# Kernel tuning notes

Hardware: AMD Instinct MI355X
Metric: run time of the kernel (lower is better)

The kernel has to match this reference:

```python
import jax, jax.numpy as jnp
import numpy as np

N_NODES = 50000
N_EDGES = 500000
D = 128
R = 8
L = 2
BN_EPS = 1e-5


def setup_inputs() -> dict:
    key = jax.random.key(0)
    ks = jax.random.split(key, 8)
    x = jax.random.normal(ks[0], (N_NODES, D), dtype=jnp.float32)
    xe = jax.random.normal(ks[1], (N_EDGES, D), dtype=jnp.float32)
    edge_index = jax.random.randint(ks[2], (2, N_EDGES), 0, N_NODES, dtype=jnp.int64)
    edge_type = jax.random.randint(ks[3], (N_EDGES,), 0, R, dtype=jnp.int64)
    # glorot init for weight/root, zeros bias; BN affine params
    w_scale = jnp.sqrt(6.0 / (D + D))
    weight = jax.random.uniform(ks[4], (L, R, D, D), jnp.float32, -w_scale, w_scale)
    root = jax.random.uniform(ks[5], (L, D, D), jnp.float32, -w_scale, w_scale)
    bias = jnp.zeros((L, D), jnp.float32)
    bn_gamma = jnp.ones((L, D), jnp.float32)
    bn_beta = jnp.zeros((L, D), jnp.float32)
    return {"x": x, "xe": xe, "edge_index": edge_index, "edge_type": edge_type,
            "weight": weight, "root": root, "bias": bias,
            "bn_gamma": bn_gamma, "bn_beta": bn_beta}


def _rgcn_edge_conv(h, xe, src, dst, etype, w, rt, b):
    # message: relu(x_j + xe) per edge (independent of relation mask)
    m = jax.nn.relu(h[src] + xe)                         # [E, D]
    # mean-aggregate per (relation, dst) via a combined segment id
    n = h.shape[0]
    seg = etype * n + dst                                # [E]
    sums = jax.ops.segment_sum(m, seg, num_segments=R * n)            # [R*N, D]
    cnt = jax.ops.segment_sum(jnp.ones((m.shape[0],), m.dtype), seg,
                              num_segments=R * n)                     # [R*N]
    mean = sums / jnp.maximum(cnt, 1.0)[:, None]
    hr = mean.reshape(R, n, -1)                          # [R, N, D]
    out = jnp.einsum('rnd,rdo->no', hr, w)               # sum_i H_i @ W_i
    out = out + h @ rt + b
    return out


def _batch_norm(h, gamma, beta):
    mu = h.mean(axis=0)
    var = jnp.mean((h - mu) ** 2, axis=0)  # biased, as torch BN (training)
    return (h - mu) * jax.lax.rsqrt(var + BN_EPS) * gamma + beta


def reference(x, xe, edge_index, edge_type, weight, root, bias, bn_gamma, bn_beta):
    src, dst = edge_index[0], edge_index[1]
    h = x
    for l in range(L):
        h = _rgcn_edge_conv(h, xe, src, dst, edge_type, weight[l], root[l], bias[l])
        h = _batch_norm(h, bn_gamma[l], bn_beta[l])
        if l != L - 1:
            h = jax.nn.relu(h)
        # drop_ratio=0 -> dropout is identity
    return h  # JK='last'
```

## Files before the change

### kernel.cpp

```cpp
#include <hip/hip_runtime.h>
#include <hip/hip_bf16.h>

typedef __attribute__((ext_vector_type(8))) short bf16x8;
typedef __attribute__((ext_vector_type(4))) float f32x4;

constexpr int D = 128;
constexpr int R = 8;
constexpr float BN_EPS = 1e-5f;

__device__ __forceinline__ unsigned short f2bf(float x) {
  __hip_bfloat16 b = __float2bfloat16(x);
  union { __hip_bfloat16 b; unsigned short u; } c; c.b = b; return c.u;
}
__device__ __forceinline__ float bf2f(unsigned short u) {
  union { float f; unsigned int i; } c; c.i = ((unsigned int)u) << 16; return c.f;
}
__device__ __forceinline__ int swz(int c) {
  return (c >> 3) * 32 + (c & 3) * 8 + ((c >> 2) & 1) * 4;
}

__global__ __launch_bounds__(256) void hist_k(const int* __restrict__ ei,
                                              const int* __restrict__ et,
                                              int* __restrict__ cnt, int E) {
  int e = blockIdx.x * 256 + threadIdx.x;
  if (e >= E) return;
  atomicAdd(&cnt[ei[E + e] * 8 + et[e]], 1);
}

__global__ __launch_bounds__(256) void scan_partial_k(const int* __restrict__ cnt,
                                                      int* __restrict__ offs,
                                                      int* __restrict__ bsum, int NK) {
  __shared__ int s[256];
  int tid = threadIdx.x;
  int base = blockIdx.x * 4096 + tid * 16;
  int loc[16];
  int sum = 0;
  #pragma unroll
  for (int i = 0; i < 16; ++i) {
    int idx = base + i;
    int v = (idx < NK) ? cnt[idx] : 0;
    loc[i] = sum; sum += v;
  }
  s[tid] = sum;
  __syncthreads();
  if (tid == 0) {
    int run = 0;
    for (int i = 0; i < 256; ++i) { int t = s[i]; s[i] = run; run += t; }
    bsum[blockIdx.x] = run;
  }
  __syncthreads();
  int off = s[tid];
  #pragma unroll
  for (int i = 0; i < 16; ++i) {
    int idx = base + i;
    if (idx < NK) offs[idx] = off + loc[i];
  }
}

__global__ void scan_bsums_k(int* __restrict__ bsum, int nb) {
  int lane = threadIdx.x;
  int carry = 0;
  for (int base = 0; base < nb; base += 64) {
    int i = base + lane;
    int orig = (i < nb) ? bsum[i] : 0;
    int v = orig;
    #pragma unroll
    for (int d = 1; d < 64; d <<= 1) {
      int t = __shfl_up(v, d, 64);
      if (lane >= d) v += t;
    }
    if (i < nb) bsum[i] = (v - orig) + carry;
    carry += __shfl(v, 63, 64);
  }
}

__global__ __launch_bounds__(256) void scan_addback_k(int* __restrict__ offs,
                                                      const int* __restrict__ bsum,
                                                      int NK, int E) {
  int idx = blockIdx.x * 256 + threadIdx.x;
  if (idx < NK) offs[idx] += bsum[idx >> 12];
  if (idx == 0) offs[NK] = E;
}

__global__ __launch_bounds__(256) void place_k(const int* __restrict__ ei,
                                               const int* __restrict__ et,
                                               const int* __restrict__ offs,
                                               int* __restrict__ cnt,
                                               int2* __restrict__ pairs, int E) {
  int e = blockIdx.x * 256 + threadIdx.x;
  if (e >= E) return;
  int key = ei[E + e] * 8 + et[e];
  int pos = offs[key] + atomicSub(&cnt[key], 1) - 1;
  pairs[pos] = make_int2(e, ei[e]);
}

__global__ __launch_bounds__(64) void bnprep_k(const float* __restrict__ cst,
                                               const float* __restrict__ gamma,
                                               const float* __restrict__ beta,
                                               float* __restrict__ sc,
                                               float* __restrict__ sh,
                                               int N, int nblk) {
  int c = blockIdx.x;
  int lane = threadIdx.x;
  float s = 0.f, q = 0.f;
  for (int b = lane; b < nblk; b += 64) {
    s += cst[(size_t)b * 256 + c];
    q += cst[(size_t)b * 256 + 128 + c];
  }
  #pragma unroll
  for (int d = 32; d >= 1; d >>= 1) {
    s += __shfl_xor(s, d, 64);
    q += __shfl_xor(q, d, 64);
  }
  if (lane == 0) {
    float invN = 1.0f / (float)N;
    float mu = s * invN;
    float var = q * invN - mu * mu;
    float scale = rsqrtf(var + BN_EPS) * gamma[c];
    sc[c] = scale;
    sh[c] = beta[c] - mu * scale;
  }
}

__device__ __forceinline__ void edge_acc(float4& acc, int e, int s, int c, int pos,
                                         const unsigned short* __restrict__ hb,
                                         const float* __restrict__ xe) {
  f32x4 xv = __builtin_nontemporal_load(((const f32x4*)xe) + (size_t)e * 32 + c);
  ushort4 hu = *(const ushort4*)(hb + (size_t)s * 128 + pos);
  acc.x += fmaxf(xv.x + bf2f(hu.x), 0.f);
  acc.y += fmaxf(xv.y + bf2f(hu.y), 0.f);
  acc.z += fmaxf(xv.z + bf2f(hu.z), 0.f);
  acc.w += fmaxf(xv.w + bf2f(hu.w), 0.f);
}

__global__ __launch_bounds__(256) void agg_k(const unsigned short* __restrict__ hb,
                                             const float* __restrict__ xe,
                                             const int2* __restrict__ pairs,
                                             const int* __restrict__ offs,
                                             unsigned short* __restrict__ Mb,
                                             int NK, int rev) {
  int grp = threadIdx.x >> 5;
  int idx = blockIdx.x * 8 + grp;
  int nIdx = NK >> 3;
  if (idx >= nIdx) return;
  if (rev) idx = nIdx - 1 - idx;
  int s0 = idx * 8;
  int c = threadIdx.x & 31;
  int pos = swz(c);

  int4 ov0 = *(const int4*)(offs + s0);
  int4 ov1 = *(const int4*)(offs + s0 + 4);
  int o8 = offs[s0 + 8];
  int st[8] = {ov0.x, ov0.y, ov0.z, ov0.w, ov1.x, ov1.y, ov1.z, ov1.w};
  int en[8] = {ov0.y, ov0.z, ov0.w, ov1.x, ov1.y, ov1.z, ov1.w, o8};

  int2 pr[8];
  #pragma unroll
  for (int j = 0; j < 8; ++j) {
    int m = en[j] - st[j];
    if (m > 0) pr[j] = pairs[st[j] + min(c, min(m, 32) - 1)];
  }

  float4 acc[8];
  #pragma unroll
  for (int j = 0; j < 8; ++j) acc[j] = make_float4(0.f, 0.f, 0.f, 0.f);

#define EP(j, i) edge_acc(acc[j], __shfl(pr[j].x, (i), 32), \
                          __shfl(pr[j].y, (i), 32), c, pos, hb, xe)

  #pragma unroll
  for (int j = 0; j < 8; ++j) {
    int m = en[j] - st[j];
    if (m > 0) {
      int mm = min(m, 32);
      EP(j, 0);
      if (mm >= 2) EP(j, 1);
      if (mm >= 3) EP(j, 2);
      if (mm >= 4) EP(j, 3);
      for (int i = 4; i < mm; ++i) EP(j, i);
      for (int base = st[j] + 32; base < en[j]; base += 32) {
        int mm2 = min(32, en[j] - base);
        int2 pr2 = pairs[base + min(c, mm2 - 1)];
        for (int i = 0; i < mm2; ++i)
          edge_acc(acc[j], __shfl(pr2.x, i, 32), __shfl(pr2.y, i, 32),
                   c, pos, hb, xe);
      }
    }
  }
#undef EP

  #pragma unroll
  for (int j = 0; j < 8; ++j) {
    int len = en[j] - st[j];
    float inv = (len > 0) ? 1.0f / (float)len : 0.f;
    ushort4 u;
    u.x = f2bf(acc[j].x * inv); u.y = f2bf(acc[j].y * inv);
    u.z = f2bf(acc[j].z * inv); u.w = f2bf(acc[j].w * inv);
    *(ushort4*)(Mb + (size_t)(s0 + j) * 128 + pos) = u;
  }
}

template <int AFF>
__global__ __launch_bounds__(256) void cast_swz_k(const float* __restrict__ in,
                                                  unsigned short* __restrict__ outb,
                                                  const float* __restrict__ sc,
                                                  const float* __restrict__ sh,
                                                  int n4) {
  int gi = blockIdx.x * 256 + threadIdx.x;
  if (gi >= n4) return;
  int n = gi >> 5, c = gi & 31;
  float4 v = ((const float4*)in)[gi];
  if (AFF) {
    float4 scv = *(const float4*)(sc + c * 4);
    float4 shv = *(const float4*)(sh + c * 4);
    v.x = fmaxf(fmaf(v.x, scv.x, shv.x), 0.f);
    v.y = fmaxf(fmaf(v.y, scv.y, shv.y), 0.f);
    v.z = fmaxf(fmaf(v.z, scv.z, shv.z), 0.f);
    v.w = fmaxf(fmaf(v.w, scv.w, shv.w), 0.f);
  }
  int pos = swz(c);
  ushort4 u;
  u.x = f2bf(v.x); u.y = f2bf(v.y); u.z = f2bf(v.z); u.w = f2bf(v.w);
  *(ushort4*)(outb + (size_t)n * 128 + pos) = u;
}

__global__ __launch_bounds__(256) void wcast_k(const float* __restrict__ W,
                                               const float* __restrict__ root,
                                               unsigned short* __restrict__ Whi) {
  int idx = blockIdx.x * 256 + threadIdx.x;
  if (idx >= 1152 * 128) return;
  int k = idx >> 7, col = idx & 127;
  float w = (k < 1024) ? W[idx] : root[idx - 1024 * 128];
  int kk = k & 31;
  int pos = (k & ~31) + ((kk & 15) >> 2) * 8 + (kk >> 4) * 4 + (kk & 3);
  Whi[col * 1152 + pos] = f2bf(w);
}

__global__ __launch_bounds__(256) void gemm_k(
    const unsigned short* __restrict__ Mb,
    const unsigned short* __restrict__ hb,
    const unsigned short* __restrict__ Whi,
    const float* __restrict__ bias,
    float* __restrict__ out,
    float* __restrict__ cst,
    int N, int rev) {
  const int tid = threadIdx.x;
  const int wv = tid >> 6, lane = tid & 63;
  const int lr = lane & 15, g = lane >> 4;
  const int bid = rev ? (gridDim.x - 1 - blockIdx.x) : blockIdx.x;
  const int r0 = bid * 128;
  const int cf0 = wv * 2;

  int row[8];
  #pragma unroll
  for (int rf = 0; rf < 8; ++rf) row[rf] = min(r0 + rf * 16 + lr, N - 1);

  const unsigned short* pb0 = Whi + (size_t)(cf0 * 16 + lr) * 1152 + g * 8;
  const unsigned short* pb1 = pb0 + 16 * 1152;

  f32x4 acc[8][2];
  #pragma unroll
  for (int a = 0; a < 8; ++a)
    #pragma unroll
    for (int b = 0; b < 2; ++b) acc[a][b] = (f32x4){0.f, 0.f, 0.f, 0.f};

  #pragma unroll 2
  for (int t = 0; t < 32; ++t) {
    bf16x8 b0 = *(const bf16x8*)(pb0 + t * 32);
    bf16x8 b1 = *(const bf16x8*)(pb1 + t * 32);
    #pragma unroll
    for (int rf = 0; rf < 8; ++rf) {
      bf16x8 a = *(const bf16x8*)(Mb + (size_t)row[rf] * 1024 + t * 32 + g * 8);
      acc[rf][0] = __builtin_amdgcn_mfma_f32_16x16x32_bf16(a, b0, acc[rf][0], 0, 0, 0);
      acc[rf][1] = __builtin_amdgcn_mfma_f32_16x16x32_bf16(a, b1, acc[rf][1], 0, 0, 0);
    }
  }
  #pragma unroll
  for (int tt = 0; tt < 4; ++tt) {
    bf16x8 b0 = *(const bf16x8*)(pb0 + 1024 + tt * 32);
    bf16x8 b1 = *(const bf16x8*)(pb1 + 1024 + tt * 32);
    #pragma unroll
    for (int rf = 0; rf < 8; ++rf) {
      bf16x8 a = *(const bf16x8*)(hb + (size_t)row[rf] * 128 + tt * 32 + g * 8);
      acc[rf][0] = __builtin_amdgcn_mfma_f32_16x16x32_bf16(a, b0, acc[rf][0], 0, 0, 0);
      acc[rf][1] = __builtin_amdgcn_mfma_f32_16x16x32_bf16(a, b1, acc[rf][1], 0, 0, 0);
    }
  }

  #pragma unroll
  for (int c = 0; c < 2; ++c) {
    int col = (cf0 + c) * 16 + lr;
    float bs = bias[col];
    float s = 0.f, q = 0.f;
    #pragma unroll
    for (int rf = 0; rf < 8; ++rf) {
      #pragma unroll
      for (int j = 0; j < 4; ++j) {
        int r = r0 + rf * 16 + g * 4 + j;
        if (r < N) {
          float v = acc[rf][c][j] + bs;
          out[(size_t)r * 128 + col] = v;
          s += v; q += v * v;
        }
      }
    }
    s += __shfl_xor(s, 16); s += __shfl_xor(s, 32);
    q += __shfl_xor(q, 16); q += __shfl_xor(q, 32);
    if (g == 0) {
      cst[(size_t)blockIdx.x * 256 + col] = s;
      cst[(size_t)blockIdx.x * 256 + 128 + col] = q;
    }
  }
}

__global__ __launch_bounds__(256) void bn_apply_k(
    const float* __restrict__ in, float* __restrict__ out,
    const float* __restrict__ sc, const float* __restrict__ sh, int N) {
  int gi = blockIdx.x * 256 + threadIdx.x;
  if (gi >= N * 32) return;
  int c0 = (gi & 31) * 4;
  float4 v = ((const float4*)in)[gi];
  float4 scv = *(const float4*)(sc + c0);
  float4 shv = *(const float4*)(sh + c0);
  float4 o;
  o.x = fmaf(v.x, scv.x, shv.x);
  o.y = fmaf(v.y, scv.y, shv.y);
  o.z = fmaf(v.z, scv.z, shv.z);
  o.w = fmaf(v.w, scv.w, shv.w);
  ((float4*)out)[gi] = o;
}

extern "C" void kernel_launch(void* const* d_in, const int* in_sizes, int n_in,
                              void* d_out, int out_size, void* d_ws, size_t ws_size,
                              hipStream_t stream) {
  const float* x      = (const float*)d_in[0];
  const float* xe     = (const float*)d_in[1];
  const int*   ei     = (const int*)d_in[2];
  const int*   et     = (const int*)d_in[3];
  const float* weight = (const float*)d_in[4];
  const float* root   = (const float*)d_in[5];
  const float* bias   = (const float*)d_in[6];
  const float* gamma  = (const float*)d_in[7];
  const float* beta   = (const float*)d_in[8];
  float* out = (float*)d_out;

  const int N = in_sizes[0] / D;
  const int E = in_sizes[3];
  const int NK = N * R;

  const int gemmBlocks = (N + 127) / 128;

  char* w = (char*)d_ws;
  size_t off = 0;
  auto alloc = [&](size_t bytes) { char* p = w + off; off = (off + bytes + 255) & ~(size_t)255; return p; };
  unsigned short* Mb   = (unsigned short*)alloc((size_t)NK * 128 * 2);
  unsigned short* hb   = (unsigned short*)alloc((size_t)N * 128 * 2);
  float*          h1   = (float*)alloc((size_t)N * 128 * 4);
  unsigned short* Whi  = (unsigned short*)alloc(1152 * 128 * 2);
  int*            offs = (int*)alloc((size_t)(NK + 8) * 4);
  int*            cnt  = (int*)alloc((size_t)NK * 4);
  int2*           pairs= (int2*)alloc((size_t)E * 8);
  int*            bsum = (int*)alloc(512 * 4);
  float*          cst0 = (float*)alloc((size_t)gemmBlocks * 256 * 4);
  float*          cst1 = (float*)alloc((size_t)gemmBlocks * 256 * 4);
  float*          sc0  = (float*)alloc(128 * 4);
  float*          sh0  = (float*)alloc(128 * 4);
  float*          sc1  = (float*)alloc(128 * 4);
  float*          sh1  = (float*)alloc(128 * 4);

  const int NB = (NK + 4095) / 4096;

  hipMemsetAsync(cnt, 0, (size_t)NK * 4, stream);
  hist_k<<<(E + 255) / 256, 256, 0, stream>>>(ei, et, cnt, E);
  scan_partial_k<<<NB, 256, 0, stream>>>(cnt, offs, bsum, NK);
  scan_bsums_k<<<1, 64, 0, stream>>>(bsum, NB);
  scan_addback_k<<<(NK + 255) / 256, 256, 0, stream>>>(offs, bsum, NK, E);
  place_k<<<(E + 255) / 256, 256, 0, stream>>>(ei, et, offs, cnt, pairs, E);

  const int aggBlocks  = ((NK >> 3) + 7) / 8;
  const int castBlocks = (N * 32 + 255) / 256;

  wcast_k<<<576, 256, 0, stream>>>(weight, root, Whi);
  cast_swz_k<0><<<castBlocks, 256, 0, stream>>>(x, hb, nullptr, nullptr, N * 32);
  agg_k<<<aggBlocks, 256, 0, stream>>>(hb, xe, pairs, offs, Mb, NK, 0);
  gemm_k<<<gemmBlocks, 256, 0, stream>>>(Mb, hb, Whi, bias, h1, cst0, N, 1);
  bnprep_k<<<128, 64, 0, stream>>>(cst0, gamma, beta, sc0, sh0, N, gemmBlocks);

  wcast_k<<<576, 256, 0, stream>>>(weight + (size_t)1024 * 128,
                                   root + (size_t)128 * 128, Whi);
  cast_swz_k<1><<<castBlocks, 256, 0, stream>>>(h1, hb, sc0, sh0, N * 32);
  agg_k<<<aggBlocks, 256, 0, stream>>>(hb, xe, pairs, offs, Mb, NK, 1);
  gemm_k<<<gemmBlocks, 256, 0, stream>>>(Mb, hb, Whi, bias + D, out, cst1, N, 0);
  bnprep_k<<<128, 64, 0, stream>>>(cst1, gamma + D, beta + D, sc1, sh1, N, gemmBlocks);
  bn_apply_k<<<castBlocks, 256, 0, stream>>>(out, out, sc1, sh1, N);
}
```

Before: 447.1 us.

## Fuse per-relation mean aggregation into GEMM via double-buffered LDS tiles

Replaces the separate aggregation kernel and GEMM with one fused kernel. For each 64-node tile, the kernel aggregates the messages of one relation into a swizzled LDS buffer while MFMA consumes the previous relation's buffer. This removes the round trip of the large intermediate Mb matrix (N*R*128 bf16) through global memory and one launch per layer. In exchange, GEMM tiles shrink from 128 to 64 rows, B fragments are reloaded more often, LDS use limits occupancy, and the irregular gather now shares waves with the MFMA work, which can cause imbalance.

```diff
diff --git a/kernel.cpp b/kernel.cpp
--- a/kernel.cpp
+++ b/kernel.cpp
@@ -131,73 +131,6 @@
   acc.y += fmaxf(xv.y + bf2f(hu.y), 0.f);
   acc.z += fmaxf(xv.z + bf2f(hu.z), 0.f);
   acc.w += fmaxf(xv.w + bf2f(hu.w), 0.f);
-}
-
-__global__ __launch_bounds__(256) void agg_k(const unsigned short* __restrict__ hb,
-                                             const float* __restrict__ xe,
-                                             const int2* __restrict__ pairs,
-                                             const int* __restrict__ offs,
-                                             unsigned short* __restrict__ Mb,
-                                             int NK, int rev) {
-  int grp = threadIdx.x >> 5;
-  int idx = blockIdx.x * 8 + grp;
-  int nIdx = NK >> 3;
-  if (idx >= nIdx) return;
-  if (rev) idx = nIdx - 1 - idx;
-  int s0 = idx * 8;
-  int c = threadIdx.x & 31;
-  int pos = swz(c);
-
-  int4 ov0 = *(const int4*)(offs + s0);
-  int4 ov1 = *(const int4*)(offs + s0 + 4);
-  int o8 = offs[s0 + 8];
-  int st[8] = {ov0.x, ov0.y, ov0.z, ov0.w, ov1.x, ov1.y, ov1.z, ov1.w};
-  int en[8] = {ov0.y, ov0.z, ov0.w, ov1.x, ov1.y, ov1.z, ov1.w, o8};
-
-  int2 pr[8];
-  #pragma unroll
-  for (int j = 0; j < 8; ++j) {
-    int m = en[j] - st[j];
-    if (m > 0) pr[j] = pairs[st[j] + min(c, min(m, 32) - 1)];
-  }
-
-  float4 acc[8];
-  #pragma unroll
-  for (int j = 0; j < 8; ++j) acc[j] = make_float4(0.f, 0.f, 0.f, 0.f);
-
-#define EP(j, i) edge_acc(acc[j], __shfl(pr[j].x, (i), 32), \
-                          __shfl(pr[j].y, (i), 32), c, pos, hb, xe)
-
-  #pragma unroll
-  for (int j = 0; j < 8; ++j) {
-    int m = en[j] - st[j];
-    if (m > 0) {
-      int mm = min(m, 32);
-      EP(j, 0);
-      if (mm >= 2) EP(j, 1);
-      if (mm >= 3) EP(j, 2);
-      if (mm >= 4) EP(j, 3);
-      for (int i = 4; i < mm; ++i) EP(j, i);
-      for (int base = st[j] + 32; base < en[j]; base += 32) {
-        int mm2 = min(32, en[j] - base);
-        int2 pr2 = pairs[base + min(c, mm2 - 1)];
-        for (int i = 0; i < mm2; ++i)
-          edge_acc(acc[j], __shfl(pr2.x, i, 32), __shfl(pr2.y, i, 32),
-                   c, pos, hb, xe);
-      }
-    }
-  }
-#undef EP
-
-  #pragma unroll
-  for (int j = 0; j < 8; ++j) {
-    int len = en[j] - st[j];
-    float inv = (len > 0) ? 1.0f / (float)len : 0.f;
-    ushort4 u;
-    u.x = f2bf(acc[j].x * inv); u.y = f2bf(acc[j].y * inv);
-    u.z = f2bf(acc[j].z * inv); u.w = f2bf(acc[j].w * inv);
-    *(ushort4*)(Mb + (size_t)(s0 + j) * 128 + pos) = u;
-  }
 }
 
 template <int AFF>
@@ -236,69 +169,145 @@
   Whi[col * 1152 + pos] = f2bf(w);
 }
 
-__global__ __launch_bounds__(256) void gemm_k(
-    const unsigned short* __restrict__ Mb,
+#define GETOFF(i) ((i)==0?ov0.x:(i)==1?ov0.y:(i)==2?ov0.z:(i)==3?ov0.w: \
+                   (i)==4?ov1.x:(i)==5?ov1.y:(i)==6?ov1.z:(i)==7?ov1.w:o8)
+
+#define AGG_PHASE(RR, BUF) do { \
+    int stc = GETOFF(RR), enc = GETOFF((RR)+1); \
+    int st[8], en[8]; \
+    _Pragma("unroll") \
+    for (int j = 0; j < 8; ++j) { st[j] = __shfl(stc, j, 32); en[j] = __shfl(enc, j, 32); } \
+    int2 pr[8]; \
+    _Pragma("unroll") \
+    for (int j = 0; j < 8; ++j) { \
+      int m = en[j] - st[j]; \
+      if (m > 0) pr[j] = pairs[st[j] + min(c, min(m, 32) - 1)]; \
+    } \
+    float4 ac[8]; \
+    _Pragma("unroll") \
+    for (int j = 0; j < 8; ++j) ac[j] = make_float4(0.f, 0.f, 0.f, 0.f); \
+    _Pragma("unroll") \
+    for (int j = 0; j < 8; ++j) { \
+      int m = en[j] - st[j]; \
+      if (m > 0) { \
+        int mm = min(m, 32); \
+        edge_acc(ac[j], __shfl(pr[j].x, 0, 32), __shfl(pr[j].y, 0, 32), c, posq, hb, xe); \
+        if (mm >= 2) edge_acc(ac[j], __shfl(pr[j].x, 1, 32), __shfl(pr[j].y, 1, 32), c, posq, hb, xe); \
+        if (mm >= 3) edge_acc(ac[j], __shfl(pr[j].x, 2, 32), __shfl(pr[j].y, 2, 32), c, posq, hb, xe); \
+        if (mm >= 4) edge_acc(ac[j], __shfl(pr[j].x, 3, 32), __shfl(pr[j].y, 3, 32), c, posq, hb, xe); \
+        for (int i = 4; i < mm; ++i) \
+          edge_acc(ac[j], __shfl(pr[j].x, i, 32), __shfl(pr[j].y, i, 32), c, posq, hb, xe); \
+        for (int b2 = st[j] + 32; b2 < en[j]; b2 += 32) { \
+          int mm2 = min(32, en[j] - b2); \
+          int2 pr2 = pairs[b2 + min(c, mm2 - 1)]; \
+          for (int i = 0; i < mm2; ++i) \
+            edge_acc(ac[j], __shfl(pr2.x, i, 32), __shfl(pr2.y, i, 32), c, posq, hb, xe); \
+        } \
+      } \
+    } \
+    _Pragma("unroll") \
+    for (int j = 0; j < 8; ++j) { \
+      int len = en[j] - st[j]; \
+      float inv = (len > 0) ? 1.0f / (float)len : 0.f; \
+      ushort4 u; \
+      u.x = f2bf(ac[j].x * inv); u.y = f2bf(ac[j].y * inv); \
+      u.z = f2bf(ac[j].z * inv); u.w = f2bf(ac[j].w * inv); \
+      int rowl = grp * 8 + j; \
+      int byte = rowl * 256 + (posb ^ ((rowl & 7) << 4)); \
+      *(ushort4*)((char*)(&Abuf[BUF][0]) + byte) = u; \
+    } \
+  } while (0)
+
+#define MFMA_PHASE(RR, BUF) do { \
+    _Pragma("unroll") \
+    for (int kt = 0; kt < 4; ++kt) { \
+      int t = (RR) * 4 + kt; \
+      bf16x8 b0 = *(const bf16x8*)(pb0 + t * 32); \
+      bf16x8 b1 = *(const bf16x8*)(pb1 + t * 32); \
+      _Pragma("unroll") \
+      for (int rf = 0; rf < 4; ++rf) { \
+        int rowl = rf * 16 + lr; \
+        int byte = rowl * 256 + (((kt * 32 + g4 * 8) * 2) ^ ((rowl & 7) << 4)); \
+        bf16x8 a = *(const bf16x8*)((const char*)(&Abuf[BUF][0]) + byte); \
+        acc[rf][0] = __builtin_amdgcn_mfma_f32_16x16x32_bf16(a, b0, acc[rf][0], 0, 0, 0); \
+        acc[rf][1] = __builtin_amdgcn_mfma_f32_16x16x32_bf16(a, b1, acc[rf][1], 0, 0, 0); \
+      } \
+    } \
+  } while (0)
+
+__global__ __launch_bounds__(256) void fused_k(
     const unsigned short* __restrict__ hb,
+    const float* __restrict__ xe,
+    const int2* __restrict__ pairs,
+    const int* __restrict__ offs,
     const unsigned short* __restrict__ Whi,
     const float* __restrict__ bias,
     float* __restrict__ out,
     float* __restrict__ cst,
     int N, int rev) {
+  __shared__ unsigned short Abuf[2][64 * 128];
   const int tid = threadIdx.x;
   const int wv = tid >> 6, lane = tid & 63;
-  const int lr = lane & 15, g = lane >> 4;
+  const int lr = lane & 15, g4 = lane >> 4;
+  const int grp = tid >> 5, c = tid & 31;
   const int bid = rev ? (gridDim.x - 1 - blockIdx.x) : blockIdx.x;
-  const int r0 = bid * 128;
+  const int r0 = bid * 64;
   const int cf0 = wv * 2;
-
-  int row[8];
-  #pragma unroll
-  for (int rf = 0; rf < 8; ++rf) row[rf] = min(r0 + rf * 16 + lr, N - 1);
-
-  const unsigned short* pb0 = Whi + (size_t)(cf0 * 16 + lr) * 1152 + g * 8;
+  const int posq = swz(c);
+  const int posb = posq * 2;
+
+  int base9 = min(r0 + grp * 8 + min(c, 7), N - 1) * 8;
+  int4 ov0 = *(const int4*)(offs + base9);
+  int4 ov1 = *(const int4*)(offs + base9 + 4);
+  int o8 = offs[base9 + 8];
+
+  const unsigned short* pb0 = Whi + (size_t)(cf0 * 16 + lr) * 1152 + g4 * 8;
   const unsigned short* pb1 = pb0 + 16 * 1152;
 
-  f32x4 acc[8][2];
-  #pragma unroll
-  for (int a = 0; a < 8; ++a)
+  f32x4 acc[4][2];
+  #pragma unroll
+  for (int a = 0; a < 4; ++a)
     #pragma unroll
     for (int b = 0; b < 2; ++b) acc[a][b] = (f32x4){0.f, 0.f, 0.f, 0.f};
 
-  #pragma unroll 2
-  for (int t = 0; t < 32; ++t) {
-    bf16x8 b0 = *(const bf16x8*)(pb0 + t * 32);
-    bf16x8 b1 = *(const bf16x8*)(pb1 + t * 32);
-    #pragma unroll
-    for (int rf = 0; rf < 8; ++rf) {
-      bf16x8 a = *(const bf16x8*)(Mb + (size_t)row[rf] * 1024 + t * 32 + g * 8);
-      acc[rf][0] = __builtin_amdgcn_mfma_f32_16x16x32_bf16(a, b0, acc[rf][0], 0, 0, 0);
-      acc[rf][1] = __builtin_amdgcn_mfma_f32_16x16x32_bf16(a, b1, acc[rf][1], 0, 0, 0);
-    }
-  }
+  AGG_PHASE(0, 0);
+  __syncthreads();
+  AGG_PHASE(1, 1); MFMA_PHASE(0, 0); __syncthreads();
+  AGG_PHASE(2, 0); MFMA_PHASE(1, 1); __syncthreads();
+  AGG_PHASE(3, 1); MFMA_PHASE(2, 0); __syncthreads();
+  AGG_PHASE(4, 0); MFMA_PHASE(3, 1); __syncthreads();
+  AGG_PHASE(5, 1); MFMA_PHASE(4, 0); __syncthreads();
+  AGG_PHASE(6, 0); MFMA_PHASE(5, 1); __syncthreads();
+  AGG_PHASE(7, 1); MFMA_PHASE(6, 0); __syncthreads();
+  MFMA_PHASE(7, 1);
+
+  int row[4];
+  #pragma unroll
+  for (int rf = 0; rf < 4; ++rf) row[rf] = min(r0 + rf * 16 + lr, N - 1);
   #pragma unroll
   for (int tt = 0; tt < 4; ++tt) {
     bf16x8 b0 = *(const bf16x8*)(pb0 + 1024 + tt * 32);
     bf16x8 b1 = *(const bf16x8*)(pb1 + 1024 + tt * 32);
     #pragma unroll
-    for (int rf = 0; rf < 8; ++rf) {
-      bf16x8 a = *(const bf16x8*)(hb + (size_t)row[rf] * 128 + tt * 32 + g * 8);
+    for (int rf = 0; rf < 4; ++rf) {
+      bf16x8 a = *(const bf16x8*)(hb + (size_t)row[rf] * 128 + tt * 32 + g4 * 8);
       acc[rf][0] = __builtin_amdgcn_mfma_f32_16x16x32_bf16(a, b0, acc[rf][0], 0, 0, 0);
       acc[rf][1] = __builtin_amdgcn_mfma_f32_16x16x32_bf16(a, b1, acc[rf][1], 0, 0, 0);
     }
   }
 
   #pragma unroll
-  for (int c = 0; c < 2; ++c) {
-    int col = (cf0 + c) * 16 + lr;
+  for (int cc = 0; cc < 2; ++cc) {
+    int col = (cf0 + cc) * 16 + lr;
     float bs = bias[col];
     float s = 0.f, q = 0.f;
     #pragma unroll
-    for (int rf = 0; rf < 8; ++rf) {
+    for (int rf = 0; rf < 4; ++rf) {
       #pragma unroll
       for (int j = 0; j < 4; ++j) {
-        int r = r0 + rf * 16 + g * 4 + j;
+        int r = r0 + rf * 16 + g4 * 4 + j;
         if (r < N) {
-          float v = acc[rf][c][j] + bs;
+          float v = acc[rf][cc][j] + bs;
           out[(size_t)r * 128 + col] = v;
           s += v; q += v * v;
         }
@@ -306,7 +315,7 @@
     }
     s += __shfl_xor(s, 16); s += __shfl_xor(s, 32);
     q += __shfl_xor(q, 16); q += __shfl_xor(q, 32);
-    if (g == 0) {
+    if (g4 == 0) {
       cst[(size_t)blockIdx.x * 256 + col] = s;
       cst[(size_t)blockIdx.x * 256 + 128 + col] = q;
     }
@@ -348,12 +357,11 @@
   const int E = in_sizes[3];
   const int NK = N * R;
 
-  const int gemmBlocks = (N + 127) / 128;
+  const int fusedBlocks = (N + 63) / 64;
 
   char* w = (char*)d_ws;
   size_t off = 0;
   auto alloc = [&](size_t bytes) { char* p = w + off; off = (off + bytes + 255) & ~(size_t)255; return p; };
-  unsigned short* Mb   = (unsigned short*)alloc((size_t)NK * 128 * 2);
   unsigned short* hb   = (unsigned short*)alloc((size_t)N * 128 * 2);
   float*          h1   = (float*)alloc((size_t)N * 128 * 4);
   unsigned short* Whi  = (unsigned short*)alloc(1152 * 128 * 2);
@@ -361,8 +369,8 @@
   int*            cnt  = (int*)alloc((size_t)NK * 4);
   int2*           pairs= (int2*)alloc((size_t)E * 8);
   int*            bsum = (int*)alloc(512 * 4);
-  float*          cst0 = (float*)alloc((size_t)gemmBlocks * 256 * 4);
-  float*          cst1 = (float*)alloc((size_t)gemmBlocks * 256 * 4);
+  float*          cst0 = (float*)alloc((size_t)fusedBlocks * 256 * 4);
+  float*          cst1 = (float*)alloc((size_t)fusedBlocks * 256 * 4);
   float*          sc0  = (float*)alloc(128 * 4);
   float*          sh0  = (float*)alloc(128 * 4);
   float*          sc1  = (float*)alloc(128 * 4);
@@ -377,20 +385,19 @@
   scan_addback_k<<<(NK + 255) / 256, 256, 0, stream>>>(offs, bsum, NK, E);
   place_k<<<(E + 255) / 256, 256, 0, stream>>>(ei, et, offs, cnt, pairs, E);
 
-  const int aggBlocks  = ((NK >> 3) + 7) / 8;
   const int castBlocks = (N * 32 + 255) / 256;
 
   wcast_k<<<576, 256, 0, stream>>>(weight, root, Whi);
   cast_swz_k<0><<<castBlocks, 256, 0, stream>>>(x, hb, nullptr, nullptr, N * 32);
-  agg_k<<<aggBlocks, 256, 0, stream>>>(hb, xe, pairs, offs, Mb, NK, 0);
-  gemm_k<<<gemmBlocks, 256, 0, stream>>>(Mb, hb, Whi, bias, h1, cst0, N, 1);
-  bnprep_k<<<128, 64, 0, stream>>>(cst0, gamma, beta, sc0, sh0, N, gemmBlocks);
+  fused_k<<<fusedBlocks, 256, 0, stream>>>(hb, xe, pairs, offs, Whi, bias,
+                                           h1, cst0, N, 0);
+  bnprep_k<<<128, 64, 0, stream>>>(cst0, gamma, beta, sc0, sh0, N, fusedBlocks);
 
   wcast_k<<<576, 256, 0, stream>>>(weight + (size_t)1024 * 128,
                                    root + (size_t)128 * 128, Whi);
   cast_swz_k<1><<<castBlocks, 256, 0, stream>>>(h1, hb, sc0, sh0, N * 32);
-  agg_k<<<aggBlocks, 256, 0, stream>>>(hb, xe, pairs, offs, Mb, NK, 1);
-  gemm_k<<<gemmBlocks, 256, 0, stream>>>(Mb, hb, Whi, bias + D, out, cst1, N, 0);
-  bnprep_k<<<128, 64, 0, stream>>>(cst1, gamma + D, beta + D, sc1, sh1, N, gemmBlocks);
+  fused_k<<<fusedBlocks, 256, 0, stream>>>(hb, xe, pairs, offs, Whi, bias + D,
+                                           out, cst1, N, 1);
+  bnprep_k<<<128, 64, 0, stream>>>(cst1, gamma + D, beta + D, sc1, sh1, N, fusedBlocks);
   bn_apply_k<<<castBlocks, 256, 0, stream>>>(out, out, sc1, sh1, N);
 }
```

Measured after the change: 558.1 us. +24.8%, slower.
